# Kernel tuning notes

Hardware: AMD Instinct MI355X
Metric: run time of the kernel (lower is better)

## Reference

```python
import jax, jax.numpy as jnp
import numpy as np

B, C_IN, T, N = 16, 64, 12, 5000
C_OUT = 64


def setup_inputs() -> dict:
    key = jax.random.key(0)
    k1, k2, k3, k4 = jax.random.split(key, 4)
    x = jax.random.normal(k1, (B, C_IN, T, N), dtype=jnp.float32)
    # normalized adjacency / graph shift operator (dense representation of the sparse filter)
    gcnconv_filter = jax.random.uniform(k2, (N, N), dtype=jnp.float32)
    weight = jax.random.normal(k3, (C_IN, C_OUT), dtype=jnp.float32) * (1.0 / np.sqrt(C_IN))
    bias = jax.random.normal(k4, (C_OUT,), dtype=jnp.float32) * 0.1
    return {"x": x, "gcnconv_filter": gcnconv_filter, "weight": weight, "bias": bias}


def reference(x, gcnconv_filter, weight, bias):
    batch_size, c_in, t, n_vertex = x.shape
    c_out = weight.shape[1]
    # faithful to torch: raw row-major reshape of [B, c_in, T, N] to [-1, c_in]
    x_flat = x.reshape(-1, c_in)                      # [B*T*N, c_in]
    h = (x_flat @ weight).reshape(n_vertex, -1)       # [N, B*T*c_out] (raw reshape)
    agg = gcnconv_filter @ h                          # spmm aggregation over vertices
    out = agg.reshape(-1, c_out) + bias               # [N*B*T, c_out]
    return out
```

## Files before the change

kernel.cpp:

```cpp
#include <hip/hip_runtime.h>

#define N_VERT 5000
#define NCOL   12288
#define KPAD   5056
#define MPAD   5120

#define G1_BLOCKS  15168
#define CVT_BLOCKS 25280

typedef float          f32x4  __attribute__((ext_vector_type(4)));
typedef unsigned short u16x4  __attribute__((ext_vector_type(4)));
typedef __bf16         bf16x8 __attribute__((ext_vector_type(8)));

__device__ __forceinline__ unsigned short f2bf(float f) {
  unsigned int u = __builtin_bit_cast(unsigned int, f);
  u += 0x7fffu + ((u >> 16) & 1u);
  return (unsigned short)(u >> 16);
}

__device__ __forceinline__ void async16(const unsigned short* g, unsigned short* l) {
  __builtin_amdgcn_global_load_lds(
      (const __attribute__((address_space(1))) unsigned int*)g,
      (__attribute__((address_space(3))) unsigned int*)l, 16, 0, 0);
}

__global__ __launch_bounds__(256) void prep(const float* __restrict__ x,
                                            const float* __restrict__ W,
                                            const float* __restrict__ F,
                                            unsigned short* __restrict__ Ht,
                                            unsigned short* __restrict__ Fb) {
  __shared__ float xt[64][68];
  __shared__ float Wl[64][68];
  const int tid = threadIdx.x;

  if (blockIdx.x >= G1_BLOCKS) {
    int idx = (blockIdx.x - G1_BLOCKS) * 256 + tid;
    int row = idx / (KPAD / 4);
    int c4  = (idx % (KPAD / 4)) * 4;
    u16x4 o;
    if (row < N_VERT && c4 < N_VERT) {
      f32x4 v = *(const f32x4*)(F + (long)row * N_VERT + c4);
      o.x = f2bf(v.x); o.y = f2bf(v.y); o.z = f2bf(v.z); o.w = f2bf(v.w);
    } else {
      o.x = 0; o.y = 0; o.z = 0; o.w = 0;
    }
    *(u16x4*)(Fb + (long)row * KPAD + c4) = o;
    return;
  }

  const int utile = blockIdx.x % 79;
  const int rr    = blockIdx.x / 79;

  for (int i = tid; i < 4096; i += 256) Wl[i >> 6][i & 63] = W[i];
  {
    int rowu = tid >> 2;
    int cb   = (tid & 3) * 16;
    long u   = (long)utile * 64 + rowu;
    bool valid = (u < N_VERT);
    const float* src = x + (u * 192 + rr) * 64;
#pragma unroll
    for (int q = 0; q < 4; ++q) {
      int col = cb + q * 4;
      f32x4 v = {0.f, 0.f, 0.f, 0.f};
      if (valid) v = *(const f32x4*)(src + col);
      xt[col + 0][rowu] = v.x;
      xt[col + 1][rowu] = v.y;
      xt[col + 2][rowu] = v.z;
      xt[col + 3][rowu] = v.w;
    }
  }
  __syncthreads();

  const int ul0 = (tid & 15) * 4;
  const int j0  = (tid >> 4) * 4;
  float acc[4][4] = {};
#pragma unroll 8
  for (int c = 0; c < 64; ++c) {
    f32x4 xv = *(const f32x4*)&xt[c][ul0];
    f32x4 wv = *(const f32x4*)&Wl[c][j0];
#pragma unroll
    for (int a = 0; a < 4; ++a)
#pragma unroll
      for (int b = 0; b < 4; ++b) acc[a][b] += xv[a] * wv[b];
  }

  long ug = (long)utile * 64 + ul0;
#pragma unroll
  for (int b = 0; b < 4; ++b) {
    long rowh = (long)rr * 64 + (j0 + b);
    u16x4 o = {f2bf(acc[0][b]), f2bf(acc[1][b]), f2bf(acc[2][b]), f2bf(acc[3][b])};
    *(u16x4*)(Ht + rowh * KPAD + ug) = o;
  }
}

__global__ __launch_bounds__(512, 2) void gemm2(const unsigned short* __restrict__ A,
                                                const unsigned short* __restrict__ Bt,
                                                const float* __restrict__ bias,
                                                float* __restrict__ out) {
  __shared__ __align__(16) unsigned short smem[65536];
  char* sm = (char*)smem;

  const int tid = threadIdx.x;
  const int l   = tid & 63;
  const int w   = tid >> 6;
  const int wr  = w >> 2;
  const int wc  = w & 3;
  const int la  = l & 15;

  const int xcd = blockIdx.x & 7;
  const int ii  = blockIdx.x >> 3;
  const int gg  = ii / 30;
  const int rmap= ii % 30;
  const long tM = (long)(gg * 5 + (rmap % 5)) * 256;
  const long tN = (long)(xcd * 6 + (rmap / 5)) * 256;

  const int  sRow  = l >> 3;
  const int  sCol8 = ((l & 7) ^ (l >> 3)) * 8;
  const unsigned short* gA2 = A  + (tM + sRow) * (size_t)KPAD + sCol8;
  const unsigned short* gB2 = Bt + (tN + sRow) * (size_t)KPAD + sCol8;

  auto stage2 = [&](int bufB, const unsigned short* g, int regionOff) {
    async16(g + (size_t)(w * 8)      * KPAD, (unsigned short*)(sm + bufB + regionOff + w * 1024));
    async16(g + (size_t)(w * 8 + 64) * KPAD, (unsigned short*)(sm + bufB + regionOff + (w + 8) * 1024));
  };

  const int cOff0 = ((l >> 4) * 16)      ^ ((l & 7) << 4);
  const int cOff1 = (64 + (l >> 4) * 16) ^ ((l & 7) << 4);
  const int aRow  = (wr * 128 + la) * 128;
  const int bRow  = 32768 + (wc * 64 + la) * 128;
  const char* pA0[2] = { sm + aRow + cOff0, sm + 65536 + aRow + cOff0 };
  const char* pA1[2] = { sm + aRow + cOff1, sm + 65536 + aRow + cOff1 };
  const char* pB0[2] = { sm + bRow + cOff0, sm + 65536 + bRow + cOff0 };
  const char* pB1[2] = { sm + bRow + cOff1, sm + 65536 + bRow + cOff1 };

  f32x4  acc[8][4] = {};
  bf16x8 af[4][2], b0[2][2], b1[2][2];

#define MFMA_Q(AI, BJ, BV)                                                        \
  _Pragma("unroll")                                                               \
  for (int ks = 0; ks < 2; ++ks)                                                  \
    _Pragma("unroll")                                                             \
    for (int i2 = 0; i2 < 4; ++i2)                                                \
      _Pragma("unroll")                                                           \
      for (int j2 = 0; j2 < 2; ++j2)                                              \
        acc[AI][BJ] = __builtin_amdgcn_mfma_f32_16x16x32_bf16(                    \
            af[i2][ks], BV[j2][ks], acc[AI][BJ], 0, 0, 0);

  auto tile = [&](int bi, int mode) {
    const int bo = bi << 16;
    const int ni = bi ^ 1;
#pragma unroll
    for (int i2 = 0; i2 < 4; ++i2) {
      af[i2][0] = *(const bf16x8*)(pA0[bi] + i2 * 2048);
      af[i2][1] = *(const bf16x8*)(pA1[bi] + i2 * 2048);
    }
#pragma unroll
    for (int j = 0; j < 2; ++j) {
      b1[j][0] = *(const bf16x8*)(pB0[bi] + (2 + j) * 2048);
      b1[j][1] = *(const bf16x8*)(pB1[bi] + (2 + j) * 2048);
    }
    __builtin_amdgcn_s_setprio(1);
    MFMA_Q(i2, j2, b0)
    MFMA_Q(i2, 2 + j2, b1)
    __builtin_amdgcn_s_setprio(0);
    __builtin_amdgcn_s_barrier();
#pragma unroll
    for (int i2 = 0; i2 < 4; ++i2) {
      af[i2][0] = *(const bf16x8*)(pA0[bi] + (4 + i2) * 2048);
      af[i2][1] = *(const bf16x8*)(pA1[bi] + (4 + i2) * 2048);
    }
    if (mode == 0) {
      stage2(bo, gB2, 32768);
      stage2(bo, gB2 + (size_t)128 * KPAD, 49152);
      gB2 += 64;
    }
    __builtin_amdgcn_s_setprio(1);
    MFMA_Q(4 + i2, j2, b0)
    __builtin_amdgcn_s_setprio(0);
    __builtin_amdgcn_s_barrier();
    if (mode == 0) {
      stage2(bo, gA2, 0);
      stage2(bo, gA2 + (size_t)128 * KPAD, 16384);
      gA2 += 64;
      asm volatile("s_waitcnt vmcnt(8)" ::: "memory");
    } else if (mode == 1) {
      asm volatile("s_waitcnt vmcnt(0)" ::: "memory");
    }
    __builtin_amdgcn_s_barrier();
    __builtin_amdgcn_sched_barrier(0);
    if (mode != 2) {
#pragma unroll
      for (int j = 0; j < 2; ++j) {
        b0[j][0] = *(const bf16x8*)(pB0[ni] + j * 2048);
        b0[j][1] = *(const bf16x8*)(pB1[ni] + j * 2048);
      }
    }
    __builtin_amdgcn_s_setprio(1);
    MFMA_Q(4 + i2, 2 + j2, b1)
    __builtin_amdgcn_s_setprio(0);
  };

  stage2(0, gB2, 32768); stage2(0, gB2 + (size_t)128 * KPAD, 49152);
  stage2(0, gA2, 0);     stage2(0, gA2 + (size_t)128 * KPAD, 16384);
  gA2 += 64; gB2 += 64;
  stage2(65536, gB2, 32768); stage2(65536, gB2 + (size_t)128 * KPAD, 49152);
  stage2(65536, gA2, 0);     stage2(65536, gA2 + (size_t)128 * KPAD, 16384);
  gA2 += 64; gB2 += 64;
  asm volatile("s_waitcnt vmcnt(8)" ::: "memory");
  __builtin_amdgcn_s_barrier();
  __builtin_amdgcn_sched_barrier(0);
#pragma unroll
  for (int j = 0; j < 2; ++j) {
    b0[j][0] = *(const bf16x8*)(pB0[0] + j * 2048);
    b0[j][1] = *(const bf16x8*)(pB1[0] + j * 2048);
  }

  for (int it = 0; it < 38; ++it) {
    tile(0, 0);
    tile(1, 0);
  }
  tile(0, 0);
  tile(1, 1);
  tile(0, 2);

#undef MFMA_Q

  float bv[4];
#pragma unroll
  for (int n = 0; n < 4; ++n) bv[n] = bias[n * 16 + la];
  const int rb = (l >> 4) * 4;
#pragma unroll
  for (int m = 0; m < 8; ++m) {
    long gm0 = tM + wr * 128 + m * 16 + rb;
#pragma unroll
    for (int rr2 = 0; rr2 < 4; ++rr2) {
      long gm = gm0 + rr2;
      if (gm < N_VERT) {
#pragma unroll
        for (int n = 0; n < 4; ++n) {
          long gn = tN + wc * 64 + n * 16 + la;
          out[gm * NCOL + gn] = acc[m][n][rr2] + bv[n];
        }
      }
    }
  }
}

extern "C" void kernel_launch(void* const* d_in, const int* in_sizes, int n_in,
                              void* d_out, int out_size, void* d_ws, size_t ws_size,
                              hipStream_t stream) {
  const float* x    = (const float*)d_in[0];
  const float* F    = (const float*)d_in[1];
  const float* W    = (const float*)d_in[2];
  const float* bias = (const float*)d_in[3];
  float* out = (float*)d_out;

  const size_t fbB = (size_t)MPAD * KPAD * 2;
  const size_t htB = (size_t)NCOL * KPAD * 2;
  if (ws_size < fbB + htB) return;

  unsigned short* Fb = (unsigned short*)d_ws;
  unsigned short* Ht = (unsigned short*)((char*)d_ws + fbB);

  prep <<<dim3(G1_BLOCKS + CVT_BLOCKS), 256, 0, stream>>>(x, W, F, Ht, Fb);
  gemm2<<<dim3(960),                    512, 0, stream>>>(Fb, Ht, bias, out);
}
```

Before: 664.7 us.

## Restructure GEMM main loop into quadrant-phased pipeline with explicit LDS waits

```diff
diff --git a/kernel.cpp b/kernel.cpp
--- a/kernel.cpp
+++ b/kernel.cpp
@@ -134,71 +134,35 @@
   const char* pB1[2] = { sm + bRow + cOff1, sm + 65536 + bRow + cOff1 };
 
   f32x4  acc[8][4] = {};
-  bf16x8 af[4][2], b0[2][2], b1[2][2];
-
-#define MFMA_Q(AI, BJ, BV)                                                        \
-  _Pragma("unroll")                                                               \
-  for (int ks = 0; ks < 2; ++ks)                                                  \
-    _Pragma("unroll")                                                             \
-    for (int i2 = 0; i2 < 4; ++i2)                                                \
-      _Pragma("unroll")                                                           \
-      for (int j2 = 0; j2 < 2; ++j2)                                              \
-        acc[AI][BJ] = __builtin_amdgcn_mfma_f32_16x16x32_bf16(                    \
-            af[i2][ks], BV[j2][ks], acc[AI][BJ], 0, 0, 0);
-
-  auto tile = [&](int bi, int mode) {
-    const int bo = bi << 16;
-    const int ni = bi ^ 1;
-#pragma unroll
-    for (int i2 = 0; i2 < 4; ++i2) {
-      af[i2][0] = *(const bf16x8*)(pA0[bi] + i2 * 2048);
-      af[i2][1] = *(const bf16x8*)(pA1[bi] + i2 * 2048);
-    }
-#pragma unroll
-    for (int j = 0; j < 2; ++j) {
-      b1[j][0] = *(const bf16x8*)(pB0[bi] + (2 + j) * 2048);
-      b1[j][1] = *(const bf16x8*)(pB1[bi] + (2 + j) * 2048);
-    }
-    __builtin_amdgcn_s_setprio(1);
-    MFMA_Q(i2, j2, b0)
-    MFMA_Q(i2, 2 + j2, b1)
-    __builtin_amdgcn_s_setprio(0);
-    __builtin_amdgcn_s_barrier();
-#pragma unroll
-    for (int i2 = 0; i2 < 4; ++i2) {
-      af[i2][0] = *(const bf16x8*)(pA0[bi] + (4 + i2) * 2048);
-      af[i2][1] = *(const bf16x8*)(pA1[bi] + (4 + i2) * 2048);
-    }
-    if (mode == 0) {
-      stage2(bo, gB2, 32768);
-      stage2(bo, gB2 + (size_t)128 * KPAD, 49152);
-      gB2 += 64;
-    }
-    __builtin_amdgcn_s_setprio(1);
-    MFMA_Q(4 + i2, j2, b0)
-    __builtin_amdgcn_s_setprio(0);
-    __builtin_amdgcn_s_barrier();
-    if (mode == 0) {
-      stage2(bo, gA2, 0);
-      stage2(bo, gA2 + (size_t)128 * KPAD, 16384);
-      gA2 += 64;
-      asm volatile("s_waitcnt vmcnt(8)" ::: "memory");
-    } else if (mode == 1) {
-      asm volatile("s_waitcnt vmcnt(0)" ::: "memory");
-    }
-    __builtin_amdgcn_s_barrier();
-    __builtin_amdgcn_sched_barrier(0);
-    if (mode != 2) {
-#pragma unroll
-      for (int j = 0; j < 2; ++j) {
-        b0[j][0] = *(const bf16x8*)(pB0[ni] + j * 2048);
-        b0[j][1] = *(const bf16x8*)(pB1[ni] + j * 2048);
-      }
-    }
-    __builtin_amdgcn_s_setprio(1);
-    MFMA_Q(4 + i2, 2 + j2, b1)
-    __builtin_amdgcn_s_setprio(0);
-  };
+  bf16x8 aR[4][2], bb[4][2];
+
+#define RD_A(BUF, MH)                                                         \
+  _Pragma("unroll")                                                           \
+  for (int i = 0; i < 4; ++i) {                                               \
+    aR[i][0] = *(const bf16x8*)(pA0[BUF] + ((MH)*4 + i) * 2048);              \
+    aR[i][1] = *(const bf16x8*)(pA1[BUF] + ((MH)*4 + i) * 2048);              \
+  }
+#define RD_B(BUF, NH)                                                         \
+  _Pragma("unroll")                                                           \
+  for (int j = 0; j < 2; ++j) {                                               \
+    bb[(NH)*2 + j][0] = *(const bf16x8*)(pB0[BUF] + ((NH)*2 + j) * 2048);     \
+    bb[(NH)*2 + j][1] = *(const bf16x8*)(pB1[BUF] + ((NH)*2 + j) * 2048);     \
+  }
+#define MM(MH, NH)                                                            \
+  __builtin_amdgcn_s_setprio(1);                                              \
+  _Pragma("unroll")                                                           \
+  for (int ks = 0; ks < 2; ++ks)                                              \
+    _Pragma("unroll")                                                         \
+    for (int i = 0; i < 4; ++i)                                               \
+      _Pragma("unroll")                                                       \
+      for (int j = 0; j < 2; ++j)                                             \
+        acc[(MH)*4 + i][(NH)*2 + j] = __builtin_amdgcn_mfma_f32_16x16x32_bf16(\
+            aR[i][ks], bb[(NH)*2 + j][ks], acc[(MH)*4 + i][(NH)*2 + j],       \
+            0, 0, 0);                                                         \
+  __builtin_amdgcn_s_setprio(0);
+#define BAR __builtin_amdgcn_s_barrier()
+#define LG0 asm volatile("s_waitcnt lgkmcnt(0)" ::: "memory")
+#define LG8 asm volatile("s_waitcnt lgkmcnt(8)" ::: "memory")
 
   stage2(0, gB2, 32768); stage2(0, gB2 + (size_t)128 * KPAD, 49152);
   stage2(0, gA2, 0);     stage2(0, gA2 + (size_t)128 * KPAD, 16384);
@@ -207,23 +171,59 @@
   stage2(65536, gA2, 0);     stage2(65536, gA2 + (size_t)128 * KPAD, 16384);
   gA2 += 64; gB2 += 64;
   asm volatile("s_waitcnt vmcnt(8)" ::: "memory");
-  __builtin_amdgcn_s_barrier();
-  __builtin_amdgcn_sched_barrier(0);
-#pragma unroll
-  for (int j = 0; j < 2; ++j) {
-    b0[j][0] = *(const bf16x8*)(pB0[0] + j * 2048);
-    b0[j][1] = *(const bf16x8*)(pB1[0] + j * 2048);
-  }
-
-  for (int it = 0; it < 38; ++it) {
-    tile(0, 0);
-    tile(1, 0);
-  }
-  tile(0, 0);
-  tile(1, 1);
-  tile(0, 2);
-
-#undef MFMA_Q
+  BAR;
+
+  auto cyc = [&](int sA12, int sB78, int drain) {
+    RD_A(0, 0); RD_B(0, 0);
+    if (sA12) stage2(65536, gA2, 0);
+    LG8;
+    BAR; LG0; MM(0, 0); BAR;
+    RD_B(0, 1);
+    if (sA12) { stage2(65536, gA2 + (size_t)128 * KPAD, 16384); gA2 += 64; }
+    BAR; LG0; MM(0, 1); BAR;
+    RD_A(0, 1);
+    stage2(0, gB2, 32768);
+    BAR; LG0; MM(1, 1); BAR;
+    stage2(0, gB2 + (size_t)128 * KPAD, 49152); gB2 += 64;
+    BAR; MM(1, 0);
+    asm volatile("s_waitcnt vmcnt(4)" ::: "memory");
+    BAR;
+    RD_A(1, 0); RD_B(1, 0);
+    stage2(0, gA2, 0);
+    LG8;
+    BAR; LG0; MM(0, 0); BAR;
+    RD_B(1, 1);
+    stage2(0, gA2 + (size_t)128 * KPAD, 16384); gA2 += 64;
+    BAR; LG0; MM(0, 1); BAR;
+    RD_A(1, 1);
+    if (sB78) stage2(65536, gB2, 32768);
+    BAR; LG0; MM(1, 1); BAR;
+    if (sB78) { stage2(65536, gB2 + (size_t)128 * KPAD, 49152); gB2 += 64; }
+    BAR; MM(1, 0);
+    if (drain) { asm volatile("s_waitcnt vmcnt(0)" ::: "memory"); }
+    else       { asm volatile("s_waitcnt vmcnt(4)" ::: "memory"); }
+    BAR;
+  };
+
+  cyc(0, 1, 0);
+#pragma unroll 1
+  for (int i = 1; i < 38; ++i) cyc(1, 1, 0);
+  cyc(1, 0, 1);
+
+  RD_A(0, 0); RD_B(0, 0);
+  BAR; LG0; MM(0, 0); BAR;
+  RD_B(0, 1);
+  BAR; LG0; MM(0, 1); BAR;
+  RD_A(0, 1);
+  BAR; LG0; MM(1, 1); BAR;
+  MM(1, 0);
+
+#undef RD_A
+#undef RD_B
+#undef MM
+#undef BAR
+#undef LG0
+#undef LG8
 
   float bv[4];
 #pragma unroll
```

Measured after the change: 686.7 us. 1.03x slower.

## Shrink GEMM tiles to 128x256 with BK=32 and 256-thread blocks

Applied to the files above, without the earlier changes.

```diff
diff --git a/kernel.cpp b/kernel.cpp
--- a/kernel.cpp
+++ b/kernel.cpp
@@ -93,137 +93,104 @@
   }
 }
 
-__global__ __launch_bounds__(512, 2) void gemm2(const unsigned short* __restrict__ A,
+__global__ __launch_bounds__(256, 2) void gemm2(const unsigned short* __restrict__ A,
                                                 const unsigned short* __restrict__ Bt,
                                                 const float* __restrict__ bias,
                                                 float* __restrict__ out) {
-  __shared__ __align__(16) unsigned short smem[65536];
+  __shared__ __align__(16) unsigned short smem[24576];
   char* sm = (char*)smem;
 
   const int tid = threadIdx.x;
   const int l   = tid & 63;
   const int w   = tid >> 6;
-  const int wr  = w >> 2;
-  const int wc  = w & 3;
   const int la  = l & 15;
 
-  const int xcd = blockIdx.x & 7;
-  const int ii  = blockIdx.x >> 3;
-  const int gg  = ii / 30;
-  const int rmap= ii % 30;
-  const long tM = (long)(gg * 5 + (rmap % 5)) * 256;
-  const long tN = (long)(xcd * 6 + (rmap / 5)) * 256;
-
-  const int  sRow  = l >> 3;
-  const int  sCol8 = ((l & 7) ^ (l >> 3)) * 8;
-  const unsigned short* gA2 = A  + (tM + sRow) * (size_t)KPAD + sCol8;
-  const unsigned short* gB2 = Bt + (tN + sRow) * (size_t)KPAD + sCol8;
-
-  auto stage2 = [&](int bufB, const unsigned short* g, int regionOff) {
-    async16(g + (size_t)(w * 8)      * KPAD, (unsigned short*)(sm + bufB + regionOff + w * 1024));
-    async16(g + (size_t)(w * 8 + 64) * KPAD, (unsigned short*)(sm + bufB + regionOff + (w + 8) * 1024));
+  const int xcd  = blockIdx.x & 7;
+  const int ii   = blockIdx.x >> 3;
+  const int mloc = ii / 48;
+  const int nt   = ii % 48;
+  const long tM  = (long)(xcd * 5 + mloc) * 128;
+  const long tN  = (long)nt * 256;
+
+  const unsigned short* gA2 = A  + (tM + (l >> 2)) * (size_t)KPAD + (l & 3) * 8;
+  const unsigned short* gB2 = Bt + (tN + (l >> 2)) * (size_t)KPAD + (l & 3) * 8;
+
+  auto stageA = [&](int bufB, const unsigned short* g) {
+    async16(g + (size_t)(w * 16)      * KPAD, (unsigned short*)(sm + bufB + w * 1024));
+    async16(g + (size_t)(w * 16 + 64) * KPAD, (unsigned short*)(sm + bufB + w * 1024 + 4096));
   };
-
-  const int cOff0 = ((l >> 4) * 16)      ^ ((l & 7) << 4);
-  const int cOff1 = (64 + (l >> 4) * 16) ^ ((l & 7) << 4);
-  const int aRow  = (wr * 128 + la) * 128;
-  const int bRow  = 32768 + (wc * 64 + la) * 128;
-  const char* pA0[2] = { sm + aRow + cOff0, sm + 65536 + aRow + cOff0 };
-  const char* pA1[2] = { sm + aRow + cOff1, sm + 65536 + aRow + cOff1 };
-  const char* pB0[2] = { sm + bRow + cOff0, sm + 65536 + bRow + cOff0 };
-  const char* pB1[2] = { sm + bRow + cOff1, sm + 65536 + bRow + cOff1 };
+  auto stageB = [&](int bufB, const unsigned short* g) {
+#pragma unroll
+    for (int q = 0; q < 4; ++q)
+      async16(g + (size_t)(w * 16 + q * 64) * KPAD,
+              (unsigned short*)(sm + bufB + 8192 + w * 1024 + q * 4096));
+  };
+
+  const int lofs = la * 64 + (l >> 4) * 16;
+  const char* pA[2] = { sm + lofs,                   sm + 24576 + lofs };
+  const char* pB[2] = { sm + 8192 + w * 4096 + lofs, sm + 24576 + 8192 + w * 4096 + lofs };
 
   f32x4  acc[8][4] = {};
-  bf16x8 af[4][2], b0[2][2], b1[2][2];
-
-#define MFMA_Q(AI, BJ, BV)                                                        \
-  _Pragma("unroll")                                                               \
-  for (int ks = 0; ks < 2; ++ks)                                                  \
-    _Pragma("unroll")                                                             \
-    for (int i2 = 0; i2 < 4; ++i2)                                                \
-      _Pragma("unroll")                                                           \
-      for (int j2 = 0; j2 < 2; ++j2)                                              \
-        acc[AI][BJ] = __builtin_amdgcn_mfma_f32_16x16x32_bf16(                    \
-            af[i2][ks], BV[j2][ks], acc[AI][BJ], 0, 0, 0);
+  bf16x8 af[4], bb[4];
+
+#define MM(MBASE, NLO, NHI)                                                   \
+  __builtin_amdgcn_s_setprio(1);                                             \
+  _Pragma("unroll")                                                          \
+  for (int m = 0; m < 4; ++m)                                                \
+    _Pragma("unroll")                                                        \
+    for (int n = (NLO); n < (NHI); ++n)                                      \
+      acc[(MBASE) + m][n] = __builtin_amdgcn_mfma_f32_16x16x32_bf16(         \
+          af[m], bb[n], acc[(MBASE) + m][n], 0, 0, 0);                       \
+  __builtin_amdgcn_s_setprio(0);
 
   auto tile = [&](int bi, int mode) {
-    const int bo = bi << 16;
+    const int bo = bi * 24576;
     const int ni = bi ^ 1;
 #pragma unroll
-    for (int i2 = 0; i2 < 4; ++i2) {
-      af[i2][0] = *(const bf16x8*)(pA0[bi] + i2 * 2048);
-      af[i2][1] = *(const bf16x8*)(pA1[bi] + i2 * 2048);
-    }
-#pragma unroll
-    for (int j = 0; j < 2; ++j) {
-      b1[j][0] = *(const bf16x8*)(pB0[bi] + (2 + j) * 2048);
-      b1[j][1] = *(const bf16x8*)(pB1[bi] + (2 + j) * 2048);
-    }
-    __builtin_amdgcn_s_setprio(1);
-    MFMA_Q(i2, j2, b0)
-    MFMA_Q(i2, 2 + j2, b1)
-    __builtin_amdgcn_s_setprio(0);
+    for (int m = 0; m < 4; ++m) af[m] = *(const bf16x8*)(pA[bi] + m * 1024);
+    bb[2] = *(const bf16x8*)(pB[bi] + 2 * 1024);
+    bb[3] = *(const bf16x8*)(pB[bi] + 3 * 1024);
+    MM(0, 0, 4)
     __builtin_amdgcn_s_barrier();
 #pragma unroll
-    for (int i2 = 0; i2 < 4; ++i2) {
-      af[i2][0] = *(const bf16x8*)(pA0[bi] + (4 + i2) * 2048);
-      af[i2][1] = *(const bf16x8*)(pA1[bi] + (4 + i2) * 2048);
-    }
-    if (mode == 0) {
-      stage2(bo, gB2, 32768);
-      stage2(bo, gB2 + (size_t)128 * KPAD, 49152);
-      gB2 += 64;
-    }
-    __builtin_amdgcn_s_setprio(1);
-    MFMA_Q(4 + i2, j2, b0)
-    __builtin_amdgcn_s_setprio(0);
+    for (int m = 0; m < 4; ++m) af[m] = *(const bf16x8*)(pA[bi] + (4 + m) * 1024);
+    if (mode == 0) { stageB(bo, gB2); gB2 += 32; }
+    MM(4, 0, 2)
     __builtin_amdgcn_s_barrier();
     if (mode == 0) {
-      stage2(bo, gA2, 0);
-      stage2(bo, gA2 + (size_t)128 * KPAD, 16384);
-      gA2 += 64;
-      asm volatile("s_waitcnt vmcnt(8)" ::: "memory");
+      stageA(bo, gA2); gA2 += 32;
+      asm volatile("s_waitcnt vmcnt(6)" ::: "memory");
     } else if (mode == 1) {
       asm volatile("s_waitcnt vmcnt(0)" ::: "memory");
     }
     __builtin_amdgcn_s_barrier();
     __builtin_amdgcn_sched_barrier(0);
     if (mode != 2) {
-#pragma unroll
-      for (int j = 0; j < 2; ++j) {
-        b0[j][0] = *(const bf16x8*)(pB0[ni] + j * 2048);
-        b0[j][1] = *(const bf16x8*)(pB1[ni] + j * 2048);
-      }
-    }
-    __builtin_amdgcn_s_setprio(1);
-    MFMA_Q(4 + i2, 2 + j2, b1)
-    __builtin_amdgcn_s_setprio(0);
+      bb[0] = *(const bf16x8*)(pB[ni] + 0);
+      bb[1] = *(const bf16x8*)(pB[ni] + 1024);
+    }
+    MM(4, 2, 4)
   };
 
-  stage2(0, gB2, 32768); stage2(0, gB2 + (size_t)128 * KPAD, 49152);
-  stage2(0, gA2, 0);     stage2(0, gA2 + (size_t)128 * KPAD, 16384);
-  gA2 += 64; gB2 += 64;
-  stage2(65536, gB2, 32768); stage2(65536, gB2 + (size_t)128 * KPAD, 49152);
-  stage2(65536, gA2, 0);     stage2(65536, gA2 + (size_t)128 * KPAD, 16384);
-  gA2 += 64; gB2 += 64;
-  asm volatile("s_waitcnt vmcnt(8)" ::: "memory");
+  stageB(0, gB2);     stageA(0, gA2);     gA2 += 32; gB2 += 32;
+  stageB(24576, gB2); stageA(24576, gA2); gA2 += 32; gB2 += 32;
+  asm volatile("s_waitcnt vmcnt(6)" ::: "memory");
   __builtin_amdgcn_s_barrier();
   __builtin_amdgcn_sched_barrier(0);
-#pragma unroll
-  for (int j = 0; j < 2; ++j) {
-    b0[j][0] = *(const bf16x8*)(pB0[0] + j * 2048);
-    b0[j][1] = *(const bf16x8*)(pB1[0] + j * 2048);
-  }
-
-  for (int it = 0; it < 38; ++it) {
+  bb[0] = *(const bf16x8*)(pB[0] + 0);
+  bb[1] = *(const bf16x8*)(pB[0] + 1024);
+
+#pragma unroll 1
+  for (int it = 0; it < 77; ++it) {
     tile(0, 0);
     tile(1, 0);
   }
   tile(0, 0);
-  tile(1, 1);
-  tile(0, 2);
-
-#undef MFMA_Q
+  tile(1, 0);
+  tile(0, 1);
+  tile(1, 2);
+
+#undef MM
 
   float bv[4];
 #pragma unroll
@@ -231,14 +198,14 @@
   const int rb = (l >> 4) * 4;
 #pragma unroll
   for (int m = 0; m < 8; ++m) {
-    long gm0 = tM + wr * 128 + m * 16 + rb;
+    long gm0 = tM + m * 16 + rb;
 #pragma unroll
     for (int rr2 = 0; rr2 < 4; ++rr2) {
       long gm = gm0 + rr2;
       if (gm < N_VERT) {
 #pragma unroll
         for (int n = 0; n < 4; ++n) {
-          long gn = tN + wc * 64 + n * 16 + la;
+          long gn = tN + w * 64 + n * 16 + la;
           out[gm * NCOL + gn] = acc[m][n][rr2] + bv[n];
         }
       }
@@ -263,5 +230,5 @@
   unsigned short* Ht = (unsigned short*)((char*)d_ws + fbB);
 
   prep <<<dim3(G1_BLOCKS + CVT_BLOCKS), 256, 0, stream>>>(x, W, F, Ht, Fb);
-  gemm2<<<dim3(960),                    512, 0, stream>>>(Fb, Ht, bias, out);
-}
+  gemm2<<<dim3(1920),                   256, 0, stream>>>(Fb, Ht, bias, out);
+}
```

Measured after the change: 941.7 us. 1.42x slower.
